# Kernel tuning notes

Hardware: AMD Instinct MI355X
Metric: run time of the kernel (lower is better)

## Reference

```python
import jax, jax.numpy as jnp
import numpy as np

H, DH = 8, 40            # heads, dim_head -> inner_dim = 320
SCALE = DH ** -0.5
B, N, M = 16, 4096, 77   # batch, query tokens (64x64 latent), text tokens
QD, CD, ID = 320, 768, H * DH


def setup_inputs() -> dict:
    key = jax.random.key(0)
    ks = jax.random.split(key, 7)
    x = jax.random.normal(ks[0], (B, N, QD), dtype=jnp.float32)
    context = jax.random.normal(ks[1], (B, M, CD), dtype=jnp.float32)
    # Linear weights stored as (in, out); torch nn.Linear has no bias for q/k/v
    Wq = jax.random.normal(ks[2], (QD, ID), dtype=jnp.float32) * (QD ** -0.5)
    Wk = jax.random.normal(ks[3], (CD, ID), dtype=jnp.float32) * (CD ** -0.5)
    Wv = jax.random.normal(ks[4], (CD, ID), dtype=jnp.float32) * (CD ** -0.5)
    Wo = jax.random.normal(ks[5], (ID, QD), dtype=jnp.float32) * (ID ** -0.5)
    bo = jnp.zeros((QD,), dtype=jnp.float32)
    return {"x": x, "context": context, "Wq": Wq, "Wk": Wk, "Wv": Wv, "Wo": Wo, "bo": bo}


def reference(x, context, Wq, Wk, Wv, Wo, bo):
    b, n, _ = x.shape
    m = context.shape[1]
    q = (x @ Wq).reshape(b, n, H, DH)        # to_q
    k = (context @ Wk).reshape(b, m, H, DH)  # to_k
    v = (context @ Wv).reshape(b, m, H, DH)  # to_v
    # full QK^T * scale (rank-bias path inactive: rank={} / is_add_rank=False)
    scores = jnp.einsum('bihd,bjhd->bhij', q, k) * SCALE  # [B,H,N,M]
    attn = jax.nn.softmax(scores, axis=-1)
    out = jnp.einsum('bhij,bjhd->bihd', attn, v).reshape(b, n, ID)
    return out @ Wo + bo  # to_out Linear; Dropout(p=0.0) is identity
```

## Files before the change

kernel.cpp:

```cpp
#include <hip/hip_runtime.h>

typedef unsigned short u16;
typedef unsigned int u32;
using short8 = __attribute__((ext_vector_type(8))) short;
using f32x4  = __attribute__((ext_vector_type(4))) float;

#define SCALE 0.15811388300841897f

__device__ __forceinline__ u16 f2bf(float f) {
  unsigned int u = __float_as_uint(f);
  u += 0x7fffu + ((u >> 16) & 1u);
  return (u16)(u >> 16);
}
__device__ __forceinline__ u32 pack2bf(float a, float b) {
  return (u32)f2bf(a) | ((u32)f2bf(b) << 16);
}


__global__ void prep_transpose(const float* __restrict__ Wq, const float* __restrict__ Wo,
                               const float* __restrict__ Wk, const float* __restrict__ Wv,
                               u16* __restrict__ wqt, u16* __restrict__ wot,
                               u16* __restrict__ wkt, u16* __restrict__ wvt) {
  __shared__ float ld[64][65];
  const int bid = blockIdx.x;
  const float* src; u16* dst; int K; float scale; int tk, tn;
  if (bid < 25)       { src = Wq; dst = wqt; K = 320; scale = SCALE; tk = bid / 5;         tn = bid % 5; }
  else if (bid < 50)  { src = Wo; dst = wot; K = 320; scale = 1.f;   tk = (bid - 25) / 5;  tn = (bid - 25) % 5; }
  else if (bid < 110) { src = Wk; dst = wkt; K = 768; scale = 1.f;   tk = (bid - 50) / 5;  tn = (bid - 50) % 5; }
  else                { src = Wv; dst = wvt; K = 768; scale = 1.f;   tk = (bid - 110) / 5; tn = (bid - 110) % 5; }
  const int c = threadIdx.x & 63, r0 = threadIdx.x >> 6;
  for (int rr = r0; rr < 64; rr += 4)
    ld[rr][c] = src[(size_t)(tk * 64 + rr) * 320 + tn * 64 + c];
  __syncthreads();
  for (int rr = r0; rr < 64; rr += 4)
    dst[(size_t)(tn * 64 + rr) * K + tk * 64 + c] = f2bf(ld[c][rr] * scale);
}

__global__ __launch_bounds__(256, 1)
void kv_mfma(const float* __restrict__ ctx,
             const u16* __restrict__ wkt, const u16* __restrict__ wvt,
             u16* __restrict__ kbf, u16* __restrict__ vt) {
  const int b = blockIdx.x, z = blockIdx.y;
  const int tid = threadIdx.x;
  const int w = tid >> 6, l = tid & 63, l16 = l & 15, lhi = l >> 4;
  __shared__ __align__(16) u16 sctx[80][776];

  for (int i = tid; i < 80 * 192; i += 256) {
    int row = i / 192, c4 = (i - row * 192) * 4;
    ushort4 u;
    if (row < 77) {
      float4 v = *reinterpret_cast<const float4*>(&ctx[(size_t)(b * 77 + row) * 768 + c4]);
      u.x = f2bf(v.x); u.y = f2bf(v.y); u.z = f2bf(v.z); u.w = f2bf(v.w);
    } else u = (ushort4){0, 0, 0, 0};
    *reinterpret_cast<ushort4*>(&sctx[row][c4]) = u;
  }
  if (z == 0) {
    for (int i = tid; i < 8 * 80 * 3; i += 256) {
      int hm = i / 3, q = i - hm * 3;
      int h = hm / 80, m = hm - h * 80;
      *reinterpret_cast<uint4*>(&kbf[(((size_t)b * 8 + h) * 80 + m) * 64 + 40 + q * 8]) = (uint4){0, 0, 0, 0};
    }
  } else {
    for (int i = tid; i < 8 * 48 * 2; i += 256) {
      int hd = i / 2, q = i - hd * 2;
      int h = hd / 48, d = hd - h * 48;
      *reinterpret_cast<uint4*>(&vt[(((size_t)b * 8 + h) * 48 + d) * 96 + 80 + q * 8]) = (uint4){0, 0, 0, 0};
    }
    for (int i = tid; i < 8 * 8 * 10; i += 256) {
      int h = i / 80, rem = i - h * 80;
      int d = 40 + rem / 10, q = rem - (rem / 10) * 10;
      *reinterpret_cast<uint4*>(&vt[(((size_t)b * 8 + h) * 48 + d) * 96 + q * 8]) = (uint4){0, 0, 0, 0};
    }
  }
  __syncthreads();

  f32x4 acc[5][5];
  #pragma unroll
  for (int rt = 0; rt < 5; ++rt)
    #pragma unroll
    for (int nt = 0; nt < 5; ++nt) acc[rt][nt] = (f32x4){0.f, 0.f, 0.f, 0.f};

  const u16* wbase = (z == 0 ? wkt : wvt) + (size_t)(w * 80) * 768;
  #pragma unroll 2
  for (int ks = 0; ks < 24; ++ks) {
    short8 af[5];
    #pragma unroll
    for (int rt = 0; rt < 5; ++rt)
      af[rt] = *reinterpret_cast<const short8*>(&sctx[rt * 16 + l16][ks * 32 + lhi * 8]);
    short8 bf[5];
    #pragma unroll
    for (int nt = 0; nt < 5; ++nt)
      bf[nt] = *reinterpret_cast<const short8*>(&wbase[(size_t)(nt * 16 + l16) * 768 + ks * 32 + lhi * 8]);
    #pragma unroll
    for (int rt = 0; rt < 5; ++rt)
      #pragma unroll
      for (int nt = 0; nt < 5; ++nt)
        acc[rt][nt] = __builtin_amdgcn_mfma_f32_16x16x32_bf16(af[rt], bf[nt], acc[rt][nt], 0, 0, 0);
  }

  if (z == 0) {
    #pragma unroll
    for (int rt = 0; rt < 5; ++rt)
      #pragma unroll
      for (int nt = 0; nt < 5; ++nt) {
        int c = w * 80 + nt * 16 + l16, h = c / 40, d = c - h * 40;
        #pragma unroll
        for (int r = 0; r < 4; ++r) {
          int m = rt * 16 + lhi * 4 + r;
          kbf[(((size_t)b * 8 + h) * 80 + m) * 64 + d] = f2bf(m < 77 ? acc[rt][nt][r] : 0.f);
        }
      }
  } else {
    #pragma unroll
    for (int rt = 0; rt < 5; ++rt)
      #pragma unroll
      for (int nt = 0; nt < 5; ++nt) {
        int c = w * 80 + nt * 16 + l16, h = c / 40, d = c - h * 40;
        #pragma unroll
        for (int r = 0; r < 4; ++r) {
          int m = rt * 16 + lhi * 4 + r;
          vt[(((size_t)b * 8 + h) * 48 + d) * 96 + m] = f2bf(m < 77 ? acc[rt][nt][r] : 0.f);
        }
      }
  }
}

__global__ __launch_bounds__(512, 4)
void fused(const float* __restrict__ x, const u16* __restrict__ wqt,
           const u16* __restrict__ kbf, const u16* __restrict__ vtp,
           const u16* __restrict__ wot, const float* __restrict__ bo,
           float* __restrict__ out) {
  const int b  = blockIdx.y;
  const int q0 = blockIdx.x * 64;
  const int tid = threadIdx.x;
  const int w   = tid >> 6;
  const int l   = tid & 63;
  const int l16 = l & 15;
  const int lhi = l >> 4;

  __shared__ __align__(16) u16 Qx[64][344];

  const int ctb = (w < 4) ? 3 * w : 2 * w + 4;
  int ctv[3];
  ctv[0] = ctb;
  ctv[1] = (ctb + 1 < 19) ? ctb + 1 : 19;
  ctv[2] = (ctb + 2 < 19) ? ctb + 2 : 19;

  const float4* xin = reinterpret_cast<const float4*>(x + (size_t)(b * 4096 + q0) * 320);
  for (int i = tid; i < 64 * 80; i += 512) {
    float4 v = xin[i];
    int row = i / 80, c4 = (i - row * 80) * 4;
    ushort4 u;
    u.x = f2bf(v.x); u.y = f2bf(v.y); u.z = f2bf(v.z); u.w = f2bf(v.w);
    *reinterpret_cast<ushort4*>(&Qx[row][c4]) = u;
  }
  for (int i = tid; i < 64 * 3; i += 512) {
    int row = i / 3, q = i - row * 3;
    *reinterpret_cast<uint4*>(&Qx[row][320 + q * 8]) = (uint4){0u, 0u, 0u, 0u};
  }
  __syncthreads();

  {
    f32x4 qacc[4][3];
    #pragma unroll
    for (int rt = 0; rt < 4; ++rt)
      #pragma unroll
      for (int nt = 0; nt < 3; ++nt) qacc[rt][nt] = (f32x4){0.f, 0.f, 0.f, 0.f};
    #pragma unroll
    for (int ks = 0; ks < 10; ++ks) {
      short8 af[4];
      #pragma unroll
      for (int rt = 0; rt < 4; ++rt)
        af[rt] = *reinterpret_cast<const short8*>(&Qx[rt * 16 + l16][ks * 32 + lhi * 8]);
      short8 bf[3];
      #pragma unroll
      for (int nt = 0; nt < 3; ++nt)
        bf[nt] = *reinterpret_cast<const short8*>(
            &wqt[(size_t)(ctv[nt] * 16 + l16) * 320 + ks * 32 + lhi * 8]);
      #pragma unroll
      for (int nt = 0; nt < 3; ++nt)
        #pragma unroll
        for (int rt = 0; rt < 4; ++rt)
          qacc[rt][nt] = __builtin_amdgcn_mfma_f32_16x16x32_bf16(af[rt], bf[nt], qacc[rt][nt], 0, 0, 0);
    }
    __syncthreads();
    #pragma unroll
    for (int nt = 0; nt < 3; ++nt) {
      int col = ctv[nt] * 16 + l16;
      #pragma unroll
      for (int rt = 0; rt < 4; ++rt)
        #pragma unroll
        for (int r = 0; r < 4; ++r)
          Qx[rt * 16 + lhi * 4 + r][col] = f2bf(qacc[rt][nt][r]);
    }
  }
  __syncthreads();

  {
    const int wq = w & 3, hg = w >> 2;
    short8 qf[4][2];
    #pragma unroll
    for (int hi4 = 0; hi4 < 4; ++hi4)
      #pragma unroll
      for (int ks = 0; ks < 2; ++ks)
        qf[hi4][ks] = *reinterpret_cast<const short8*>(
            &Qx[wq * 16 + l16][(hg * 4 + hi4) * 40 + ks * 32 + lhi * 8]);

    const int srcLo = ((lhi & 1) << 5) + l16;
    const int srcHi = srcLo + 16;
    const bool hiSel = (lhi >= 2);

    for (int hi4 = 0; hi4 < 4; ++hi4) {
      const int h = hg * 4 + hi4;
      const u16* kh = kbf + (size_t)(b * 8 + h) * 80 * 64;
      const u16* vh = vtp + (size_t)(b * 8 + h) * 48 * 96;
      f32x4 sacc[5];
      #pragma unroll
      for (int mt = 0; mt < 5; ++mt) sacc[mt] = (f32x4){0.f, 0.f, 0.f, 0.f};
      #pragma unroll
      for (int ks = 0; ks < 2; ++ks) {
        #pragma unroll
        for (int mt = 0; mt < 5; ++mt) {
          short8 ka = *reinterpret_cast<const short8*>(&kh[(mt * 16 + l16) * 64 + ks * 32 + lhi * 8]);
          sacc[mt] = __builtin_amdgcn_mfma_f32_16x16x32_bf16(ka, qf[hi4][ks], sacc[mt], 0, 0, 0);
        }
      }
      float psum = 0.f;
      #pragma unroll
      for (int mt = 0; mt < 5; ++mt)
        #pragma unroll
        for (int r = 0; r < 4; ++r) {
          float e = __expf(sacc[mt][r]);
          if (mt == 4 && lhi * 4 + r >= 13) e = 0.f;
          sacc[mt][r] = e;
          psum += e;
        }
      psum += __shfl_xor(psum, 16);
      psum += __shfl_xor(psum, 32);
      float rs = 1.f / psum;
      u32 pk[5][2];
      #pragma unroll
      for (int mt = 0; mt < 5; ++mt) {
        pk[mt][0] = pack2bf(sacc[mt][0] * rs, sacc[mt][1] * rs);
        pk[mt][1] = pack2bf(sacc[mt][2] * rs, sacc[mt][3] * rs);
      }
      uint4 fr[3];
      #pragma unroll
      for (int ks = 0; ks < 2; ++ks) {
        const int mtA = 2 * ks, mtB = 2 * ks + 1;
        u32 a0 = (u32)__shfl((int)pk[mtA][0], srcLo);
        u32 a1 = (u32)__shfl((int)pk[mtA][1], srcLo);
        u32 a2 = (u32)__shfl((int)pk[mtA][0], srcHi);
        u32 a3 = (u32)__shfl((int)pk[mtA][1], srcHi);
        u32 b0 = (u32)__shfl((int)pk[mtB][0], srcLo);
        u32 b1 = (u32)__shfl((int)pk[mtB][1], srcLo);
        u32 b2 = (u32)__shfl((int)pk[mtB][0], srcHi);
        u32 b3 = (u32)__shfl((int)pk[mtB][1], srcHi);
        fr[ks] = (uint4){hiSel ? b0 : a0, hiSel ? b1 : a1, hiSel ? b2 : a2, hiSel ? b3 : a3};
      }
      {
        u32 a0 = (u32)__shfl((int)pk[4][0], srcLo);
        u32 a1 = (u32)__shfl((int)pk[4][1], srcLo);
        u32 a2 = (u32)__shfl((int)pk[4][0], srcHi);
        u32 a3 = (u32)__shfl((int)pk[4][1], srcHi);
        fr[2] = (uint4){hiSel ? 0u : a0, hiSel ? 0u : a1, hiSel ? 0u : a2, hiSel ? 0u : a3};
      }
      f32x4 oacc[3];
      #pragma unroll
      for (int nt = 0; nt < 3; ++nt) oacc[nt] = (f32x4){0.f, 0.f, 0.f, 0.f};
      #pragma unroll
      for (int ks = 0; ks < 3; ++ks) {
        union { uint4 u; short8 s; } cv;
        cv.u = fr[ks];
        #pragma unroll
        for (int nt = 0; nt < 3; ++nt) {
          short8 bb = *reinterpret_cast<const short8*>(&vh[(nt * 16 + l16) * 96 + ks * 32 + lhi * 8]);
          oacc[nt] = __builtin_amdgcn_mfma_f32_16x16x32_bf16(cv.s, bb, oacc[nt], 0, 0, 0);
        }
      }
      #pragma unroll
      for (int nt = 0; nt < 3; ++nt) {
        int d = nt * 16 + l16;
        if (d < 40) {
          #pragma unroll
          for (int r = 0; r < 4; ++r)
            Qx[wq * 16 + lhi * 4 + r][h * 40 + d] = f2bf(oacc[nt][r]);
        }
      }
    }
  }
  __syncthreads();

  {
    const int w2 = w >> 2, w4 = w & 3;
    f32x4 cacc[2][5];
    #pragma unroll
    for (int rt = 0; rt < 2; ++rt)
      #pragma unroll
      for (int nt = 0; nt < 5; ++nt) cacc[rt][nt] = (f32x4){0.f, 0.f, 0.f, 0.f};
    #pragma unroll
    for (int ks = 0; ks < 10; ++ks) {
      short8 af[2];
      #pragma unroll
      for (int rt = 0; rt < 2; ++rt)
        af[rt] = *reinterpret_cast<const short8*>(&Qx[w2 * 32 + rt * 16 + l16][ks * 32 + lhi * 8]);
      #pragma unroll
      for (int nt = 0; nt < 5; ++nt) {
        short8 bf = *reinterpret_cast<const short8*>(
            &wot[(size_t)(w4 * 80 + nt * 16 + l16) * 320 + ks * 32 + lhi * 8]);
        #pragma unroll
        for (int rt = 0; rt < 2; ++rt)
          cacc[rt][nt] = __builtin_amdgcn_mfma_f32_16x16x32_bf16(af[rt], bf, cacc[rt][nt], 0, 0, 0);
      }
    }
    #pragma unroll
    for (int nt = 0; nt < 5; ++nt) {
      int col = w4 * 80 + nt * 16 + l16;
      float bias = bo[col];
      #pragma unroll
      for (int rt = 0; rt < 2; ++rt) {
        #pragma unroll
        for (int r = 0; r < 4; ++r) {
          int row = w2 * 32 + rt * 16 + lhi * 4 + r;
          out[(size_t)(b * 4096 + q0 + row) * 320 + col] = cacc[rt][nt][r] + bias;
        }
      }
    }
  }
}

extern "C" void kernel_launch(void* const* d_in, const int* in_sizes, int n_in,
                              void* d_out, int out_size, void* d_ws, size_t ws_size,
                              hipStream_t stream) {
  (void)in_sizes; (void)n_in; (void)out_size; (void)ws_size;
  const float* x       = (const float*)d_in[0];
  const float* context = (const float*)d_in[1];
  const float* Wq      = (const float*)d_in[2];
  const float* Wk      = (const float*)d_in[3];
  const float* Wv      = (const float*)d_in[4];
  const float* Wo      = (const float*)d_in[5];
  const float* bo      = (const float*)d_in[6];
  float* out = (float*)d_out;
  u16* ws = (u16*)d_ws;
  u16* wqt = ws;
  u16* wot = ws + 102400;
  u16* wkt = ws + 204800;
  u16* wvt = ws + 450560;
  u16* kbf = ws + 696320;
  u16* vtp = ws + 1351680;

  prep_transpose<<<170, 256, 0, stream>>>(Wq, Wo, Wk, Wv, wqt, wot, wkt, wvt);
  kv_mfma<<<dim3(16, 2), 256, 0, stream>>>(context, wkt, wvt, kbf, vtp);
  fused<<<dim3(64, 16), 512, 0, stream>>>(x, wqt, kbf, vtp, wot, bo, out);
}
```

Baseline: 189.4 us.

## Halve fused block to 4 waves with larger per-wave tiles

The fused kernel now runs with 256 threads (4 waves) instead of 512. Each wave computes 5 Q column tiles and handles all 8 heads for its 16 query rows, where before the heads were split across two wave groups. In the output projection each wave now covers all 64 rows. The Q/K fragment loads move inside the head loop, and an explicit lgkmcnt wait plus a sched barrier are added before the LDS writeback. The intent is to get more work and reuse per wave and less imbalance in the Q-projection split, at the cost of more registers (launch bounds 256,3) and fewer waves per block to hide latency.

```diff
diff --git a/kernel.cpp b/kernel.cpp
--- a/kernel.cpp
+++ b/kernel.cpp
@@ -125,7 +125,7 @@
   }
 }
 
-__global__ __launch_bounds__(512, 4)
+__global__ __launch_bounds__(256, 3)
 void fused(const float* __restrict__ x, const u16* __restrict__ wqt,
            const u16* __restrict__ kbf, const u16* __restrict__ vtp,
            const u16* __restrict__ wot, const float* __restrict__ bo,
@@ -140,53 +140,45 @@
 
   __shared__ __align__(16) u16 Qx[64][344];
 
-  const int ctb = (w < 4) ? 3 * w : 2 * w + 4;
-  int ctv[3];
-  ctv[0] = ctb;
-  ctv[1] = (ctb + 1 < 19) ? ctb + 1 : 19;
-  ctv[2] = (ctb + 2 < 19) ? ctb + 2 : 19;
-
   const float4* xin = reinterpret_cast<const float4*>(x + (size_t)(b * 4096 + q0) * 320);
-  for (int i = tid; i < 64 * 80; i += 512) {
+  for (int i = tid; i < 64 * 80; i += 256) {
     float4 v = xin[i];
     int row = i / 80, c4 = (i - row * 80) * 4;
     ushort4 u;
     u.x = f2bf(v.x); u.y = f2bf(v.y); u.z = f2bf(v.z); u.w = f2bf(v.w);
     *reinterpret_cast<ushort4*>(&Qx[row][c4]) = u;
   }
-  for (int i = tid; i < 64 * 3; i += 512) {
+  for (int i = tid; i < 64 * 3; i += 256) {
     int row = i / 3, q = i - row * 3;
     *reinterpret_cast<uint4*>(&Qx[row][320 + q * 8]) = (uint4){0u, 0u, 0u, 0u};
   }
   __syncthreads();
 
   {
-    f32x4 qacc[4][3];
+    f32x4 qacc[4][5];
     #pragma unroll
     for (int rt = 0; rt < 4; ++rt)
       #pragma unroll
-      for (int nt = 0; nt < 3; ++nt) qacc[rt][nt] = (f32x4){0.f, 0.f, 0.f, 0.f};
+      for (int nt = 0; nt < 5; ++nt) qacc[rt][nt] = (f32x4){0.f, 0.f, 0.f, 0.f};
     #pragma unroll
     for (int ks = 0; ks < 10; ++ks) {
       short8 af[4];
       #pragma unroll
       for (int rt = 0; rt < 4; ++rt)
         af[rt] = *reinterpret_cast<const short8*>(&Qx[rt * 16 + l16][ks * 32 + lhi * 8]);
-      short8 bf[3];
-      #pragma unroll
-      for (int nt = 0; nt < 3; ++nt)
-        bf[nt] = *reinterpret_cast<const short8*>(
-            &wqt[(size_t)(ctv[nt] * 16 + l16) * 320 + ks * 32 + lhi * 8]);
-      #pragma unroll
-      for (int nt = 0; nt < 3; ++nt)
+      #pragma unroll
+      for (int nt = 0; nt < 5; ++nt) {
+        short8 bf = *reinterpret_cast<const short8*>(
+            &wqt[(size_t)((w * 5 + nt) * 16 + l16) * 320 + ks * 32 + lhi * 8]);
         #pragma unroll
         for (int rt = 0; rt < 4; ++rt)
-          qacc[rt][nt] = __builtin_amdgcn_mfma_f32_16x16x32_bf16(af[rt], bf[nt], qacc[rt][nt], 0, 0, 0);
+          qacc[rt][nt] = __builtin_amdgcn_mfma_f32_16x16x32_bf16(af[rt], bf, qacc[rt][nt], 0, 0, 0);
+      }
     }
     __syncthreads();
     #pragma unroll
-    for (int nt = 0; nt < 3; ++nt) {
-      int col = ctv[nt] * 16 + l16;
+    for (int nt = 0; nt < 5; ++nt) {
+      int col = (w * 5 + nt) * 16 + l16;
       #pragma unroll
       for (int rt = 0; rt < 4; ++rt)
         #pragma unroll
@@ -197,33 +189,24 @@
   __syncthreads();
 
   {
-    const int wq = w & 3, hg = w >> 2;
-    short8 qf[4][2];
-    #pragma unroll
-    for (int hi4 = 0; hi4 < 4; ++hi4)
-      #pragma unroll
-      for (int ks = 0; ks < 2; ++ks)
-        qf[hi4][ks] = *reinterpret_cast<const short8*>(
-            &Qx[wq * 16 + l16][(hg * 4 + hi4) * 40 + ks * 32 + lhi * 8]);
-
     const int srcLo = ((lhi & 1) << 5) + l16;
     const int srcHi = srcLo + 16;
     const bool hiSel = (lhi >= 2);
 
-    for (int hi4 = 0; hi4 < 4; ++hi4) {
-      const int h = hg * 4 + hi4;
+    for (int h = 0; h < 8; ++h) {
       const u16* kh = kbf + (size_t)(b * 8 + h) * 80 * 64;
       const u16* vh = vtp + (size_t)(b * 8 + h) * 48 * 96;
+      short8 qk0 = *reinterpret_cast<const short8*>(&Qx[w * 16 + l16][h * 40 + lhi * 8]);
+      short8 qk1 = *reinterpret_cast<const short8*>(&Qx[w * 16 + l16][h * 40 + 32 + lhi * 8]);
       f32x4 sacc[5];
       #pragma unroll
       for (int mt = 0; mt < 5; ++mt) sacc[mt] = (f32x4){0.f, 0.f, 0.f, 0.f};
       #pragma unroll
-      for (int ks = 0; ks < 2; ++ks) {
-        #pragma unroll
-        for (int mt = 0; mt < 5; ++mt) {
-          short8 ka = *reinterpret_cast<const short8*>(&kh[(mt * 16 + l16) * 64 + ks * 32 + lhi * 8]);
-          sacc[mt] = __builtin_amdgcn_mfma_f32_16x16x32_bf16(ka, qf[hi4][ks], sacc[mt], 0, 0, 0);
-        }
+      for (int mt = 0; mt < 5; ++mt) {
+        short8 ka0 = *reinterpret_cast<const short8*>(&kh[(mt * 16 + l16) * 64 + lhi * 8]);
+        sacc[mt] = __builtin_amdgcn_mfma_f32_16x16x32_bf16(ka0, qk0, sacc[mt], 0, 0, 0);
+        short8 ka1 = *reinterpret_cast<const short8*>(&kh[(mt * 16 + l16) * 64 + 32 + lhi * 8]);
+        sacc[mt] = __builtin_amdgcn_mfma_f32_16x16x32_bf16(ka1, qk1, sacc[mt], 0, 0, 0);
       }
       float psum = 0.f;
       #pragma unroll
@@ -278,13 +261,15 @@
           oacc[nt] = __builtin_amdgcn_mfma_f32_16x16x32_bf16(cv.s, bb, oacc[nt], 0, 0, 0);
         }
       }
+      asm volatile("s_waitcnt lgkmcnt(0)" ::: "memory");
+      __builtin_amdgcn_sched_barrier(0);
       #pragma unroll
       for (int nt = 0; nt < 3; ++nt) {
         int d = nt * 16 + l16;
         if (d < 40) {
           #pragma unroll
           for (int r = 0; r < 4; ++r)
-            Qx[wq * 16 + lhi * 4 + r][h * 40 + d] = f2bf(oacc[nt][r]);
+            Qx[w * 16 + lhi * 4 + r][h * 40 + d] = f2bf(oacc[nt][r]);
         }
       }
     }
@@ -292,36 +277,35 @@
   __syncthreads();
 
   {
-    const int w2 = w >> 2, w4 = w & 3;
-    f32x4 cacc[2][5];
-    #pragma unroll
-    for (int rt = 0; rt < 2; ++rt)
+    f32x4 cacc[4][5];
+    #pragma unroll
+    for (int rt = 0; rt < 4; ++rt)
       #pragma unroll
       for (int nt = 0; nt < 5; ++nt) cacc[rt][nt] = (f32x4){0.f, 0.f, 0.f, 0.f};
     #pragma unroll
     for (int ks = 0; ks < 10; ++ks) {
-      short8 af[2];
-      #pragma unroll
-      for (int rt = 0; rt < 2; ++rt)
-        af[rt] = *reinterpret_cast<const short8*>(&Qx[w2 * 32 + rt * 16 + l16][ks * 32 + lhi * 8]);
+      short8 af[4];
+      #pragma unroll
+      for (int rt = 0; rt < 4; ++rt)
+        af[rt] = *reinterpret_cast<const short8*>(&Qx[rt * 16 + l16][ks * 32 + lhi * 8]);
       #pragma unroll
       for (int nt = 0; nt < 5; ++nt) {
         short8 bf = *reinterpret_cast<const short8*>(
-            &wot[(size_t)(w4 * 80 + nt * 16 + l16) * 320 + ks * 32 + lhi * 8]);
-        #pragma unroll
-        for (int rt = 0; rt < 2; ++rt)
+            &wot[(size_t)(w * 80 + nt * 16 + l16) * 320 + ks * 32 + lhi * 8]);
+        #pragma unroll
+        for (int rt = 0; rt < 4; ++rt)
           cacc[rt][nt] = __builtin_amdgcn_mfma_f32_16x16x32_bf16(af[rt], bf, cacc[rt][nt], 0, 0, 0);
       }
     }
     #pragma unroll
     for (int nt = 0; nt < 5; ++nt) {
-      int col = w4 * 80 + nt * 16 + l16;
+      int col = w * 80 + nt * 16 + l16;
       float bias = bo[col];
       #pragma unroll
-      for (int rt = 0; rt < 2; ++rt) {
+      for (int rt = 0; rt < 4; ++rt) {
         #pragma unroll
         for (int r = 0; r < 4; ++r) {
-          int row = w2 * 32 + rt * 16 + lhi * 4 + r;
+          int row = rt * 16 + lhi * 4 + r;
           out[(size_t)(b * 4096 + q0 + row) * 320 + col] = cacc[rt][nt][r] + bias;
         }
       }
@@ -351,5 +335,5 @@
 
   prep_transpose<<<170, 256, 0, stream>>>(Wq, Wo, Wk, Wv, wqt, wot, wkt, wvt);
   kv_mfma<<<dim3(16, 2), 256, 0, stream>>>(context, wkt, wvt, kbf, vtp);
-  fused<<<dim3(64, 16), 512, 0, stream>>>(x, wqt, kbf, vtp, wot, bo, out);
-}
+  fused<<<dim3(64, 16), 256, 0, stream>>>(x, wqt, kbf, vtp, wot, bo, out);
+}
```

Measured after the change: 190.3 us. Within noise of the previous version (+0.5%).

## Prefetch next head's K fragments, add MFMA priority, remap blocks across batches

Applied to the files above, without the earlier changes.

The attention loop now double-buffers the first K-slice fragments of the next head in registers while computing the current head, and loads Q fragments from shared memory per head instead of holding all of them up front. MFMA sections are wrapped in s_setprio to favor matrix issue over other waves. The grid is flattened to 1D with a block-to-(batch, query tile) mapping that interleaves batches, which changes how work is spread across XCDs and caches. The costs are more register pressure from the prefetch buffer and some extra shared-memory reads.

```diff
diff --git a/kernel.cpp b/kernel.cpp
--- a/kernel.cpp
+++ b/kernel.cpp
@@ -130,13 +130,15 @@
            const u16* __restrict__ kbf, const u16* __restrict__ vtp,
            const u16* __restrict__ wot, const float* __restrict__ bo,
            float* __restrict__ out) {
-  const int b  = blockIdx.y;
-  const int q0 = blockIdx.x * 64;
+  const int bid = blockIdx.x;
+  const int b  = (bid & 7) + 8 * ((bid >> 3) & 1);
+  const int q0 = (bid >> 4) * 64;
   const int tid = threadIdx.x;
   const int w   = tid >> 6;
   const int l   = tid & 63;
   const int l16 = l & 15;
   const int lhi = l >> 4;
+  const int w2 = w >> 2, w4 = w & 3;
 
   __shared__ __align__(16) u16 Qx[64][344];
 
@@ -198,33 +200,43 @@
 
   {
     const int wq = w & 3, hg = w >> 2;
-    short8 qf[4][2];
-    #pragma unroll
-    for (int hi4 = 0; hi4 < 4; ++hi4)
-      #pragma unroll
-      for (int ks = 0; ks < 2; ++ks)
-        qf[hi4][ks] = *reinterpret_cast<const short8*>(
-            &Qx[wq * 16 + l16][(hg * 4 + hi4) * 40 + ks * 32 + lhi * 8]);
-
     const int srcLo = ((lhi & 1) << 5) + l16;
     const int srcHi = srcLo + 16;
     const bool hiSel = (lhi >= 2);
 
+    short8 kbuf[2][5];
+    {
+      const u16* kh0 = kbf + (size_t)(b * 8 + hg * 4) * 80 * 64;
+      #pragma unroll
+      for (int mt = 0; mt < 5; ++mt)
+        kbuf[0][mt] = *reinterpret_cast<const short8*>(&kh0[(mt * 16 + l16) * 64 + lhi * 8]);
+    }
+
+    #pragma unroll
     for (int hi4 = 0; hi4 < 4; ++hi4) {
       const int h = hg * 4 + hi4;
+      const int cur = hi4 & 1;
       const u16* kh = kbf + (size_t)(b * 8 + h) * 80 * 64;
       const u16* vh = vtp + (size_t)(b * 8 + h) * 48 * 96;
+      if (hi4 < 3) {
+        const u16* khn = kh + 80 * 64;
+        #pragma unroll
+        for (int mt = 0; mt < 5; ++mt)
+          kbuf[cur ^ 1][mt] = *reinterpret_cast<const short8*>(&khn[(mt * 16 + l16) * 64 + lhi * 8]);
+      }
+      short8 qk0 = *reinterpret_cast<const short8*>(&Qx[wq * 16 + l16][h * 40 + lhi * 8]);
+      short8 qk1 = *reinterpret_cast<const short8*>(&Qx[wq * 16 + l16][h * 40 + 32 + lhi * 8]);
       f32x4 sacc[5];
       #pragma unroll
       for (int mt = 0; mt < 5; ++mt) sacc[mt] = (f32x4){0.f, 0.f, 0.f, 0.f};
-      #pragma unroll
-      for (int ks = 0; ks < 2; ++ks) {
-        #pragma unroll
-        for (int mt = 0; mt < 5; ++mt) {
-          short8 ka = *reinterpret_cast<const short8*>(&kh[(mt * 16 + l16) * 64 + ks * 32 + lhi * 8]);
-          sacc[mt] = __builtin_amdgcn_mfma_f32_16x16x32_bf16(ka, qf[hi4][ks], sacc[mt], 0, 0, 0);
-        }
-      }
+      __builtin_amdgcn_s_setprio(1);
+      #pragma unroll
+      for (int mt = 0; mt < 5; ++mt) {
+        sacc[mt] = __builtin_amdgcn_mfma_f32_16x16x32_bf16(kbuf[cur][mt], qk0, sacc[mt], 0, 0, 0);
+        short8 ka1 = *reinterpret_cast<const short8*>(&kh[(mt * 16 + l16) * 64 + 32 + lhi * 8]);
+        sacc[mt] = __builtin_amdgcn_mfma_f32_16x16x32_bf16(ka1, qk1, sacc[mt], 0, 0, 0);
+      }
+      __builtin_amdgcn_s_setprio(0);
       float psum = 0.f;
       #pragma unroll
       for (int mt = 0; mt < 5; ++mt)
@@ -268,6 +280,7 @@
       f32x4 oacc[3];
       #pragma unroll
       for (int nt = 0; nt < 3; ++nt) oacc[nt] = (f32x4){0.f, 0.f, 0.f, 0.f};
+      __builtin_amdgcn_s_setprio(1);
       #pragma unroll
       for (int ks = 0; ks < 3; ++ks) {
         union { uint4 u; short8 s; } cv;
@@ -278,6 +291,7 @@
           oacc[nt] = __builtin_amdgcn_mfma_f32_16x16x32_bf16(cv.s, bb, oacc[nt], 0, 0, 0);
         }
       }
+      __builtin_amdgcn_s_setprio(0);
       #pragma unroll
       for (int nt = 0; nt < 3; ++nt) {
         int d = nt * 16 + l16;
@@ -292,7 +306,6 @@
   __syncthreads();
 
   {
-    const int w2 = w >> 2, w4 = w & 3;
     f32x4 cacc[2][5];
     #pragma unroll
     for (int rt = 0; rt < 2; ++rt)
@@ -351,5 +364,5 @@
 
   prep_transpose<<<170, 256, 0, stream>>>(Wq, Wo, Wk, Wv, wqt, wot, wkt, wvt);
   kv_mfma<<<dim3(16, 2), 256, 0, stream>>>(context, wkt, wvt, kbf, vtp);
-  fused<<<dim3(64, 16), 512, 0, stream>>>(x, wqt, kbf, vtp, wot, bo, out);
-}
+  fused<<<1024, 512, 0, stream>>>(x, wqt, kbf, vtp, wot, bo, out);
+}
```

Result: no change. 186.6 us (-1.5%).
